# Kernel tuning notes

Measured on AMD Instinct MI355X. Metric: run time of the kernel, lower is better.

The kernel has to match this reference:

```python
import jax, jax.numpy as jnp
import numpy as np

TAU = 2.0
THR = 0.5
ALPHA = 4.0  # Sigmoid_Grad surrogate sharpness
EPS = 1e-5
HEADS = 16
SCALE = 0.25

@jax.custom_vjp
def spike(v):
    return (v > 0.0).astype(v.dtype)

def _spike_fwd(v):
    return (v > 0.0).astype(v.dtype), v

def _spike_bwd(v, g):
    s = jax.nn.sigmoid(ALPHA * v)
    return (g * ALPHA * s * (1.0 - s),)

spike.defvjp(_spike_fwd, _spike_bwd)

def lif(x):
    # x: (T, ...) ; stateful LIF over leading time dim, hard reset (detached spike)
    def step(mem, xt):
        mem = mem + (xt - mem) / TAU
        s = spike(mem - THR)
        mem = mem * (1.0 - jax.lax.stop_gradient(s))
        return mem, s
    _, s = jax.lax.scan(step, jnp.zeros_like(x[0]), x)
    return s

def bn(x, p):
    # x: (T,B,C,N), p: (4,C) = (gamma, beta, mean, var); inference-form BatchNorm1d
    g, b, m, v = p
    shp = (1, 1, -1, 1)
    return (x - m.reshape(shp)) * (g.reshape(shp) / jnp.sqrt(v.reshape(shp) + EPS)) + b.reshape(shp)

def conv_bn_lif(x, w, p, bias=None):
    # 1x1 Conv1d == channel matmul: (T,B,Cin,N) x (Cout,Cin) -> (T,B,Cout,N)
    y = jnp.einsum('tbcn,oc->tbon', x, w)
    if bias is not None:
        y = y + bias.reshape(1, 1, -1, 1)
    return lif(bn(y, p))

def _block(x, q_w, q_bn, k_w, k_bn, v_w, v_bn, proj_w, proj_bn,
           fc1_w, fc1_b, fc1_bn, fc2_w, fc2_b, fc2_bn):
    T, B, C, N = x.shape
    D = C // HEADS

    def to_heads(y):  # (T,B,C,N) -> (T,B,H,N,D)
        return y.transpose(0, 1, 3, 2).reshape(T, B, N, HEADS, D).transpose(0, 1, 3, 2, 4)

    q = to_heads(conv_bn_lif(x, q_w, q_bn))
    k = to_heads(conv_bn_lif(x, k_w, k_bn))
    v = to_heads(conv_bn_lif(x, v_w, v_bn))

    attn = jnp.einsum('tbhnd,tbhmd->tbhnm', q, k) * SCALE  # no softmax
    r = jnp.einsum('tbhnm,tbhmd->tbhnd', attn, v) * SCALE
    r = r.transpose(0, 1, 2, 4, 3).reshape(T, B, C, N)  # (T,B,H,D,N) -> (T,B,C,N)
    r = lif(r)  # attn_lif
    attn_out = conv_bn_lif(r, proj_w, proj_bn)  # proj conv+bn+lif

    x = x + attn_out  # residual 1

    h = conv_bn_lif(x, fc1_w, fc1_bn, fc1_b)
    m = conv_bn_lif(h, fc2_w, fc2_bn, fc2_b)
    return x + m  # residual 2

def setup_inputs() -> dict:
    key = jax.random.key(0)
    ks = jax.random.split(key, 16)
    T, B, C, N = 4, 16, 256, 512
    H = 1024  # mlp hidden = 4*C
    w = 0.05
    d = {}
    d['x'] = jax.random.normal(ks[0], (T, B, C, N), jnp.float32)
    d['q_w'] = jax.random.normal(ks[1], (C, C), jnp.float32) * w
    d['q_bn'] = jax.random.uniform(ks[2], (4, C), jnp.float32, 0.5, 1.5)
    d['k_w'] = jax.random.normal(ks[3], (C, C), jnp.float32) * w
    d['k_bn'] = jax.random.uniform(ks[4], (4, C), jnp.float32, 0.5, 1.5)
    d['v_w'] = jax.random.normal(ks[5], (C, C), jnp.float32) * w
    d['v_bn'] = jax.random.uniform(ks[6], (4, C), jnp.float32, 0.5, 1.5)
    d['proj_w'] = jax.random.normal(ks[7], (C, C), jnp.float32) * w
    d['proj_bn'] = jax.random.uniform(ks[8], (4, C), jnp.float32, 0.5, 1.5)
    d['fc1_w'] = jax.random.normal(ks[9], (H, C), jnp.float32) * w
    d['fc1_b'] = jnp.zeros((H,), jnp.float32)
    d['fc1_bn'] = jax.random.uniform(ks[10], (4, H), jnp.float32, 0.5, 1.5)
    d['fc2_w'] = jax.random.normal(ks[11], (C, H), jnp.float32) * w
    d['fc2_b'] = jnp.zeros((C,), jnp.float32)
    d['fc2_bn'] = jax.random.uniform(ks[12], (4, C), jnp.float32, 0.5, 1.5)
    return d

def reference(x, q_w, q_bn, k_w, k_bn, v_w, v_bn, proj_w, proj_bn,
              fc1_w, fc1_b, fc1_bn, fc2_w, fc2_b, fc2_bn):
    return _block(x, q_w, q_bn, k_w, k_bn, v_w, v_bn, proj_w, proj_bn,
                  fc1_w, fc1_b, fc1_bn, fc2_w, fc2_b, fc2_bn)
```

## Files before the change

kernel.cpp:

```cpp
#include <hip/hip_runtime.h>

#pragma clang fp contract(off)

typedef unsigned char u8;
typedef unsigned int u32;

#define TSTEPS 4

template <int P, int BK, int XMODE, bool HASX2, int OMODE>
__global__ __launch_bounds__(256) void conv_bn_lif(
    const void* __restrict__ X1v, const u8* __restrict__ X2,
    const float* __restrict__ Wt, const float* __restrict__ bias,
    const float* __restrict__ bnp,
    u8* __restrict__ Sout,
    const float* __restrict__ Xres, const u8* __restrict__ AOres,
    float* __restrict__ Fout,
    int Bsz, int Cin, int Cout, int N)
{
  constexpr int BO   = 16 * P;
  constexpr int BN   = 128;
  constexpr int TPR  = 256 / BK;
  constexpr int FPT  = BN / TPR;
  constexpr int NF4  = FPT / 4;
  constexpr int THRO = 256 / BO;
  constexpr int WPAD = (P == 4) ? 4 : 0;
  constexpr int XROWF = BN + 8;

  const int tid = threadIdx.x;
  const int tx = tid & 15, ty = tid >> 4;
  const int nBase = blockIdx.x * BN, oBase = blockIdx.y * BO, b = blockIdx.z;
  const int KT = Cin / BK;
  const int TT = TSTEPS * KT;

  __shared__ __align__(16) float Ws[2][BK][BO + WPAD];
  __shared__ __align__(16) u8 Xraw[(XMODE == 0) ? (2 * BK * XROWF * 4)
                                                : (2 * BK * BN)];
  __shared__ __align__(16) float BnL[BO][4];

  float* XF = (float*)Xraw;
  u8*    X8 = Xraw;

  if (tid < BO) {
    int o = oBase + tid;
    float g  = bnp[0 * Cout + o];
    float be = bnp[1 * Cout + o];
    float m  = bnp[2 * Cout + o];
    float vv = bnp[3 * Cout + o];
    float d_f = (float)((double)vv + (double)1e-5f);
    float s_f = (float)sqrt((double)d_f);
    BnL[tid][0] = (float)((double)g / (double)s_f);
    BnL[tid][1] = m;
    BnL[tid][2] = be;
    BnL[tid][3] = bias ? bias[o] : 0.0f;
  }

  float mem[P][8], acc[P][8];
  #pragma unroll
  for (int p = 0; p < P; ++p)
    #pragma unroll
    for (int q = 0; q < 8; ++q) { mem[p][q] = 0.0f; acc[p][q] = 0.0f; }

  const int xRow = tid / TPR;
  const int xcF  = (tid % TPR) * FPT;
  const int wO   = tid / THRO;
  const int wK   = (tid % THRO) * 8;

  float4 px[NF4];
  u32    pxu[NF4];
  u32    pau[NF4];
  float4 pwa, pwb;

  auto issue = [&](int i) {
    const int tI = i / KT, k0 = (i % KT) * BK;
    const size_t xb = (size_t)(tI * Bsz + b) * Cin * N
                    + (size_t)(k0 + xRow) * N + nBase + xcF;
    if constexpr (XMODE == 0) {
      const float* xp = (const float*)X1v + xb;
      #pragma unroll
      for (int f = 0; f < NF4; ++f) px[f] = *(const float4*)(xp + 4 * f);
    } else {
      const u8* xp = (const u8*)X1v + xb;
      if constexpr (NF4 == 4) {
        uint4 u = *(const uint4*)xp;
        pxu[0] = u.x; pxu[1] = u.y; pxu[2] = u.z; pxu[3] = u.w;
      } else {
        uint2 u = *(const uint2*)xp;
        pxu[0] = u.x; pxu[1] = u.y;
      }
    }
    if constexpr (HASX2) {
      const u8* ap = X2 + xb;
      if constexpr (NF4 == 4) {
        uint4 u = *(const uint4*)ap;
        pau[0] = u.x; pau[1] = u.y; pau[2] = u.z; pau[3] = u.w;
      } else {
        uint2 u = *(const uint2*)ap;
        pau[0] = u.x; pau[1] = u.y;
      }
    }
    const size_t wb = (size_t)(oBase + wO) * Cin + k0 + wK;
    pwa = *(const float4*)(Wt + wb);
    pwb = *(const float4*)(Wt + wb + 4);
  };

  auto commit = [&](int bf) {
    if constexpr (XMODE == 0) {
      #pragma unroll
      for (int f = 0; f < NF4; ++f) {
        float4 v = px[f];
        if constexpr (HASX2) {
          u32 a2 = pau[f];
          v.x = v.x + (float)(a2 & 0xffu);
          v.y = v.y + (float)((a2 >> 8) & 0xffu);
          v.z = v.z + (float)((a2 >> 16) & 0xffu);
          v.w = v.w + (float)((a2 >> 24) & 0xffu);
        }
        *(float4*)&XF[((size_t)(bf * BK + xRow)) * XROWF + xcF + 4 * f] = v;
      }
    } else {
      if constexpr (NF4 == 4) {
        *(uint4*)&X8[(size_t)(bf * BK + xRow) * BN + xcF] =
            make_uint4(pxu[0], pxu[1], pxu[2], pxu[3]);
      } else {
        *(uint2*)&X8[(size_t)(bf * BK + xRow) * BN + xcF] =
            make_uint2(pxu[0], pxu[1]);
      }
    }
    Ws[bf][wK + 0][wO] = pwa.x;  Ws[bf][wK + 1][wO] = pwa.y;
    Ws[bf][wK + 2][wO] = pwa.z;  Ws[bf][wK + 3][wO] = pwa.w;
    Ws[bf][wK + 4][wO] = pwb.x;  Ws[bf][wK + 5][wO] = pwb.y;
    Ws[bf][wK + 6][wO] = pwb.z;  Ws[bf][wK + 7][wO] = pwb.w;
  };

  issue(0);
  commit(0);
  __syncthreads();

  for (int tt = 0; tt < TT; ++tt) {
    const int buf = tt & 1;
    if (tt + 1 < TT) issue(tt + 1);

    #pragma unroll
    for (int kk = 0; kk < BK; ++kk) {
      float xa[8];
      if constexpr (XMODE == 0) {
        float4 x0 = *(const float4*)&XF[(size_t)(buf * BK + kk) * XROWF + tx * 4];
        float4 x1 = *(const float4*)&XF[(size_t)(buf * BK + kk) * XROWF + 64 + tx * 4];
        xa[0] = x0.x; xa[1] = x0.y; xa[2] = x0.z; xa[3] = x0.w;
        xa[4] = x1.x; xa[5] = x1.y; xa[6] = x1.z; xa[7] = x1.w;
      } else {
        uint2 u = *(const uint2*)&X8[(size_t)(buf * BK + kk) * BN + tx * 8];
        #pragma unroll
        for (int j = 0; j < 4; ++j) xa[j]     = (float)((u.x >> (8 * j)) & 0xffu);
        #pragma unroll
        for (int j = 0; j < 4; ++j) xa[4 + j] = (float)((u.y >> (8 * j)) & 0xffu);
      }
      float wa[P];
      float4 w0 = *(const float4*)&Ws[buf][kk][ty * P];
      wa[0] = w0.x; wa[1] = w0.y; wa[2] = w0.z; wa[3] = w0.w;
      if constexpr (P == 8) {
        float4 w1 = *(const float4*)&Ws[buf][kk][ty * P + 4];
        wa[4] = w1.x; wa[5] = w1.y; wa[6] = w1.z; wa[7] = w1.w;
      }
      #pragma unroll
      for (int p = 0; p < P; ++p)
        #pragma unroll
        for (int q = 0; q < 8; ++q)
          acc[p][q] = fmaf(wa[p], xa[q], acc[p][q]);
    }

    if ((tt % KT) == KT - 1) {
      const int t = tt / KT;
      const size_t sbase = (size_t)(t * Bsz + b) * Cout * N;
      #pragma unroll
      for (int p = 0; p < P; ++p) {
        const int o = oBase + ty * P + p;
        float4 bv = *(const float4*)&BnL[ty * P + p][0];
        bool spk[8];
        #pragma unroll
        for (int q = 0; q < 8; ++q) {
          float y = acc[p][q];
          if (bias) y = y + bv.w;
          float t1 = y - bv.y;
          float t2 = t1 * bv.x;
          y = t2 + bv.z;
          float m2 = mem[p][q];
          float dd = y - m2;
          m2 = m2 + dd * 0.5f;
          bool sp = (m2 - 0.5f) > 0.0f;
          mem[p][q] = sp ? 0.0f : m2;
          spk[q] = sp;
          acc[p][q] = 0.0f;
        }
        if constexpr (XMODE == 0) {
          const size_t rb0 = sbase + (size_t)o * N + nBase + tx * 4;
          u32 pk0 = 0, pk1 = 0;
          #pragma unroll
          for (int j = 0; j < 4; ++j) {
            if (spk[j])     pk0 |= (1u << (8 * j));
            if (spk[4 + j]) pk1 |= (1u << (8 * j));
          }
          *(u32*)&Sout[rb0]      = pk0;
          *(u32*)&Sout[rb0 + 64] = pk1;
        } else {
          const size_t rb = sbase + (size_t)o * N + nBase + tx * 8;
          if constexpr (OMODE == 0) {
            u32 pk0 = 0, pk1 = 0;
            #pragma unroll
            for (int j = 0; j < 4; ++j) {
              if (spk[j])     pk0 |= (1u << (8 * j));
              if (spk[4 + j]) pk1 |= (1u << (8 * j));
            }
            *(uint2*)&Sout[rb] = make_uint2(pk0, pk1);
          } else {
            float4 xr0 = *(const float4*)&Xres[rb];
            float4 xr1 = *(const float4*)&Xres[rb + 4];
            uint2 av = *(const uint2*)&AOres[rb];
            float xa4[8] = {xr0.x, xr0.y, xr0.z, xr0.w,
                            xr1.x, xr1.y, xr1.z, xr1.w};
            float o4[8];
            #pragma unroll
            for (int j = 0; j < 4; ++j) {
              float s = spk[j] ? 1.0f : 0.0f;
              float xn = xa4[j] + (float)((av.x >> (8 * j)) & 0xffu);
              o4[j] = xn + s;
            }
            #pragma unroll
            for (int j = 0; j < 4; ++j) {
              float s = spk[4 + j] ? 1.0f : 0.0f;
              float xn = xa4[4 + j] + (float)((av.y >> (8 * j)) & 0xffu);
              o4[4 + j] = xn + s;
            }
            *(float4*)&Fout[rb]     = make_float4(o4[0], o4[1], o4[2], o4[3]);
            *(float4*)&Fout[rb + 4] = make_float4(o4[4], o4[5], o4[6], o4[7]);
          }
        }
      }
    }

    __syncthreads();
    if (tt + 1 < TT) commit((tt + 1) & 1);
    __syncthreads();
  }
}

__global__ __launch_bounds__(256) void attn_lif(
    const u8* __restrict__ Qs, const u8* __restrict__ Ks,
    const u8* __restrict__ Vs, u8* __restrict__ Rs,
    int Bsz, int C, int N)
{
  const int tid = threadIdx.x;
  const int h = blockIdx.x & 15;
  const int b = blockIdx.x >> 4;

  __shared__ u8 qs[16][528];
  __shared__ u8 ks[16][528];
  __shared__ u8 vs[16][528];
  __shared__ int Gs[16][17];

  const int eG = tid >> 4;
  const int dG = tid & 15;
  const int dR = tid >> 4;
  const int nR0 = tid & 15;

  float mem[32];
  #pragma unroll
  for (int i = 0; i < 32; ++i) mem[i] = 0.0f;

  for (int t = 0; t < TSTEPS; ++t) {
    __syncthreads();
    const size_t base = ((size_t)(t * Bsz + b) * C + h * 16) * N;
    for (int i = 0; i < 32; ++i) {
      int flat = tid + 256 * i;
      int d = flat >> 9, n = flat & 511;
      size_t g = base + (size_t)d * N + n;
      qs[d][n] = Qs[g];
      ks[d][n] = Ks[g];
      vs[d][n] = Vs[g];
    }
    __syncthreads();

    int gi = 0;
    for (int n = 0; n < 512; ++n)
      gi += (int)ks[eG][n] * (int)vs[dG][n];
    Gs[eG][dG] = gi;
    __syncthreads();

    int Greg[16];
    #pragma unroll
    for (int e = 0; e < 16; ++e) Greg[e] = Gs[e][dR];

    const size_t obase = ((size_t)(t * Bsz + b) * C + h * 16 + dR) * N;
    for (int j = 0; j < 32; ++j) {
      int n = nR0 + 16 * j;
      int ri = 0;
      #pragma unroll
      for (int e = 0; e < 16; ++e)
        ri += qs[e][n] ? Greg[e] : 0;
      float r = (float)ri * 0.0625f;
      float m2 = mem[j];
      float d = r - m2;
      m2 = m2 + d * 0.5f;
      float s = (m2 - 0.5f) > 0.0f ? 1.0f : 0.0f;
      mem[j] = (s > 0.0f) ? 0.0f : m2;
      Rs[obase + n] = (s > 0.0f) ? (u8)1 : (u8)0;
    }
  }
}

extern "C" void kernel_launch(void* const* d_in, const int* in_sizes, int n_in,
                              void* d_out, int out_size, void* d_ws, size_t ws_size,
                              hipStream_t stream)
{
  const float* x     = (const float*)d_in[0];
  const float* q_w   = (const float*)d_in[1];
  const float* q_bn  = (const float*)d_in[2];
  const float* k_w   = (const float*)d_in[3];
  const float* k_bn  = (const float*)d_in[4];
  const float* v_w   = (const float*)d_in[5];
  const float* v_bn  = (const float*)d_in[6];
  const float* p_w   = (const float*)d_in[7];
  const float* p_bn  = (const float*)d_in[8];
  const float* f1_w  = (const float*)d_in[9];
  const float* f1_b  = (const float*)d_in[10];
  const float* f1_bn = (const float*)d_in[11];
  const float* f2_w  = (const float*)d_in[12];
  const float* f2_b  = (const float*)d_in[13];
  const float* f2_bn = (const float*)d_in[14];

  const int T = 4, B = 16, C = 256, N = 512, Hm = 1024;
  const size_t SZ = (size_t)T * B * C * N;

  char* ws = (char*)d_ws;
  u8* q_s  = (u8*)(ws + 0 * SZ);
  u8* k_s  = (u8*)(ws + 1 * SZ);
  u8* v_s  = (u8*)(ws + 2 * SZ);
  u8* r_s  = (u8*)(ws + 3 * SZ);
  u8* ao_s = (u8*)(ws + 4 * SZ);
  u8* h_s  = (u8*)(ws + 0 * SZ);

  dim3 blk(256);
  dim3 gC64(N / 128, C / 64, B);
  dim3 gF1(N / 128, Hm / 64, B);

  conv_bn_lif<4, 32, 0, false, 0><<<gC64, blk, 0, stream>>>(
      x, nullptr, q_w, nullptr, q_bn, q_s, nullptr, nullptr, nullptr, B, C, C, N);
  conv_bn_lif<4, 32, 0, false, 0><<<gC64, blk, 0, stream>>>(
      x, nullptr, k_w, nullptr, k_bn, k_s, nullptr, nullptr, nullptr, B, C, C, N);
  conv_bn_lif<4, 32, 0, false, 0><<<gC64, blk, 0, stream>>>(
      x, nullptr, v_w, nullptr, v_bn, v_s, nullptr, nullptr, nullptr, B, C, C, N);

  attn_lif<<<dim3(B * 16), blk, 0, stream>>>(q_s, k_s, v_s, r_s, B, C, N);

  conv_bn_lif<4, 32, 1, false, 0><<<gC64, blk, 0, stream>>>(
      r_s, nullptr, p_w, nullptr, p_bn, ao_s, nullptr, nullptr, nullptr, B, C, C, N);
  conv_bn_lif<4, 32, 0, true, 0><<<gF1, blk, 0, stream>>>(
      x, ao_s, f1_w, f1_b, f1_bn, h_s, nullptr, nullptr, nullptr, B, C, Hm, N);
  conv_bn_lif<4, 32, 1, false, 1><<<gC64, blk, 0, stream>>>(
      h_s, nullptr, f2_w, f2_b, f2_bn, nullptr, x, ao_s, (float*)d_out, B, Hm, C, N);
}
```

Measured before the change: 1.050 ms.

## Fuse Q/K/V conv launches and retune per-layer output tile sizes

Merges the three Q, K and V conv+BN+LIF launches into one grid that picks its weight, BN and output pointers from blockIdx.y. This removes two launch gaps and gives the GPU more blocks at once. It also generalises the weight loader so each layer can use its own output-channel tile: P=2 for the proj and fc2 convs to double their block count, and P=8 for fc1 to raise per-thread work. The cost is more template variants, extra runtime pointer selects, and possibly lower arithmetic intensity on the P=2 layers.

```diff
diff --git a/kernel.cpp b/kernel.cpp
--- a/kernel.cpp
+++ b/kernel.cpp
@@ -7,12 +7,14 @@
 
 #define TSTEPS 4
 
-template <int P, int BK, int XMODE, bool HASX2, int OMODE>
+template <int P, int BK, int XMODE, bool HASX2, int OMODE, int NSEL>
 __global__ __launch_bounds__(256) void conv_bn_lif(
     const void* __restrict__ X1v, const u8* __restrict__ X2,
-    const float* __restrict__ Wt, const float* __restrict__ bias,
-    const float* __restrict__ bnp,
-    u8* __restrict__ Sout,
+    const float* __restrict__ W0, const float* __restrict__ W1,
+    const float* __restrict__ W2, const float* __restrict__ bias,
+    const float* __restrict__ bn0, const float* __restrict__ bn1,
+    const float* __restrict__ bn2,
+    u8* __restrict__ S0, u8* __restrict__ S1, u8* __restrict__ S2,
     const float* __restrict__ Xres, const u8* __restrict__ AOres,
     float* __restrict__ Fout,
     int Bsz, int Cin, int Cout, int N)
@@ -22,17 +24,35 @@
   constexpr int TPR  = 256 / BK;
   constexpr int FPT  = BN / TPR;
   constexpr int NF4  = FPT / 4;
-  constexpr int THRO = 256 / BO;
-  constexpr int WPAD = (P == 4) ? 4 : 0;
+  static_assert(NF4 == 4, "loader assumes 16 elems/thread");
+  constexpr int WPT  = BO * BK / 256;
+  constexpr int NW4  = WPT / 4;
+  constexpr int TPW  = BK / WPT;
+  constexpr int WPAD = (P == 4) ? 4 : (P == 2) ? 2 : 0;
+  constexpr int WROW = BO + WPAD;
   constexpr int XROWF = BN + 8;
 
   const int tid = threadIdx.x;
   const int tx = tid & 15, ty = tid >> 4;
-  const int nBase = blockIdx.x * BN, oBase = blockIdx.y * BO, b = blockIdx.z;
+  const int nBase = blockIdx.x * BN, b = blockIdx.z;
+
+  int sel, oBase;
+  if constexpr (NSEL == 3) {
+    const int oT = gridDim.y / 3;
+    sel = blockIdx.y / oT;
+    oBase = (blockIdx.y - sel * oT) * BO;
+  } else {
+    sel = 0;
+    oBase = blockIdx.y * BO;
+  }
+  const float* __restrict__ Wt  = (sel == 0) ? W0 : (sel == 1) ? W1 : W2;
+  const float* __restrict__ bnp = (sel == 0) ? bn0 : (sel == 1) ? bn1 : bn2;
+  u8* __restrict__ Sout         = (sel == 0) ? S0 : (sel == 1) ? S1 : S2;
+
   const int KT = Cin / BK;
   const int TT = TSTEPS * KT;
 
-  __shared__ __align__(16) float Ws[2][BK][BO + WPAD];
+  __shared__ __align__(16) float Ws[2][BK][WROW];
   __shared__ __align__(16) u8 Xraw[(XMODE == 0) ? (2 * BK * XROWF * 4)
                                                 : (2 * BK * BN)];
   __shared__ __align__(16) float BnL[BO][4];
@@ -62,13 +82,13 @@
 
   const int xRow = tid / TPR;
   const int xcF  = (tid % TPR) * FPT;
-  const int wO   = tid / THRO;
-  const int wK   = (tid % THRO) * 8;
+  const int wO   = tid / TPW;
+  const int wK   = (tid % TPW) * WPT;
 
   float4 px[NF4];
   u32    pxu[NF4];
   u32    pau[NF4];
-  float4 pwa, pwb;
+  float4 pw[NW4];
 
   auto issue = [&](int i) {
     const int tI = i / KT, k0 = (i % KT) * BK;
@@ -79,28 +99,16 @@
       #pragma unroll
       for (int f = 0; f < NF4; ++f) px[f] = *(const float4*)(xp + 4 * f);
     } else {
-      const u8* xp = (const u8*)X1v + xb;
-      if constexpr (NF4 == 4) {
-        uint4 u = *(const uint4*)xp;
-        pxu[0] = u.x; pxu[1] = u.y; pxu[2] = u.z; pxu[3] = u.w;
-      } else {
-        uint2 u = *(const uint2*)xp;
-        pxu[0] = u.x; pxu[1] = u.y;
-      }
+      uint4 u = *(const uint4*)((const u8*)X1v + xb);
+      pxu[0] = u.x; pxu[1] = u.y; pxu[2] = u.z; pxu[3] = u.w;
     }
     if constexpr (HASX2) {
-      const u8* ap = X2 + xb;
-      if constexpr (NF4 == 4) {
-        uint4 u = *(const uint4*)ap;
-        pau[0] = u.x; pau[1] = u.y; pau[2] = u.z; pau[3] = u.w;
-      } else {
-        uint2 u = *(const uint2*)ap;
-        pau[0] = u.x; pau[1] = u.y;
-      }
+      uint4 u = *(const uint4*)(X2 + xb);
+      pau[0] = u.x; pau[1] = u.y; pau[2] = u.z; pau[3] = u.w;
     }
     const size_t wb = (size_t)(oBase + wO) * Cin + k0 + wK;
-    pwa = *(const float4*)(Wt + wb);
-    pwb = *(const float4*)(Wt + wb + 4);
+    #pragma unroll
+    for (int f = 0; f < NW4; ++f) pw[f] = *(const float4*)(Wt + wb + 4 * f);
   };
 
   auto commit = [&](int bf) {
@@ -118,18 +126,16 @@
         *(float4*)&XF[((size_t)(bf * BK + xRow)) * XROWF + xcF + 4 * f] = v;
       }
     } else {
-      if constexpr (NF4 == 4) {
-        *(uint4*)&X8[(size_t)(bf * BK + xRow) * BN + xcF] =
-            make_uint4(pxu[0], pxu[1], pxu[2], pxu[3]);
-      } else {
-        *(uint2*)&X8[(size_t)(bf * BK + xRow) * BN + xcF] =
-            make_uint2(pxu[0], pxu[1]);
-      }
-    }
-    Ws[bf][wK + 0][wO] = pwa.x;  Ws[bf][wK + 1][wO] = pwa.y;
-    Ws[bf][wK + 2][wO] = pwa.z;  Ws[bf][wK + 3][wO] = pwa.w;
-    Ws[bf][wK + 4][wO] = pwb.x;  Ws[bf][wK + 5][wO] = pwb.y;
-    Ws[bf][wK + 6][wO] = pwb.z;  Ws[bf][wK + 7][wO] = pwb.w;
+      *(uint4*)&X8[(size_t)(bf * BK + xRow) * BN + xcF] =
+          make_uint4(pxu[0], pxu[1], pxu[2], pxu[3]);
+    }
+    #pragma unroll
+    for (int f = 0; f < NW4; ++f) {
+      Ws[bf][wK + 4 * f + 0][wO] = pw[f].x;
+      Ws[bf][wK + 4 * f + 1][wO] = pw[f].y;
+      Ws[bf][wK + 4 * f + 2][wO] = pw[f].z;
+      Ws[bf][wK + 4 * f + 3][wO] = pw[f].w;
+    }
   };
 
   issue(0);
@@ -156,11 +162,16 @@
         for (int j = 0; j < 4; ++j) xa[4 + j] = (float)((u.y >> (8 * j)) & 0xffu);
       }
       float wa[P];
-      float4 w0 = *(const float4*)&Ws[buf][kk][ty * P];
-      wa[0] = w0.x; wa[1] = w0.y; wa[2] = w0.z; wa[3] = w0.w;
-      if constexpr (P == 8) {
-        float4 w1 = *(const float4*)&Ws[buf][kk][ty * P + 4];
-        wa[4] = w1.x; wa[5] = w1.y; wa[6] = w1.z; wa[7] = w1.w;
+      if constexpr (P == 2) {
+        float2 w0 = *(const float2*)&Ws[buf][kk][ty * 2];
+        wa[0] = w0.x; wa[1] = w0.y;
+      } else {
+        float4 w0 = *(const float4*)&Ws[buf][kk][ty * P];
+        wa[0] = w0.x; wa[1] = w0.y; wa[2] = w0.z; wa[3] = w0.w;
+        if constexpr (P == 8) {
+          float4 w1 = *(const float4*)&Ws[buf][kk][ty * P + 4];
+          wa[4] = w1.x; wa[5] = w1.y; wa[6] = w1.z; wa[7] = w1.w;
+        }
       }
       #pragma unroll
       for (int p = 0; p < P; ++p)
@@ -340,22 +351,23 @@
   u8* h_s  = (u8*)(ws + 0 * SZ);
 
   dim3 blk(256);
-  dim3 gC64(N / 128, C / 64, B);
-  dim3 gF1(N / 128, Hm / 64, B);
-
-  conv_bn_lif<4, 32, 0, false, 0><<<gC64, blk, 0, stream>>>(
-      x, nullptr, q_w, nullptr, q_bn, q_s, nullptr, nullptr, nullptr, B, C, C, N);
-  conv_bn_lif<4, 32, 0, false, 0><<<gC64, blk, 0, stream>>>(
-      x, nullptr, k_w, nullptr, k_bn, k_s, nullptr, nullptr, nullptr, B, C, C, N);
-  conv_bn_lif<4, 32, 0, false, 0><<<gC64, blk, 0, stream>>>(
-      x, nullptr, v_w, nullptr, v_bn, v_s, nullptr, nullptr, nullptr, B, C, C, N);
+  dim3 gQKV(N / 128, 3 * (C / 64), B);
+  dim3 gP2(N / 128, C / 32, B);
+  dim3 gF1(N / 128, Hm / 128, B);
+
+  conv_bn_lif<4, 32, 0, false, 0, 3><<<gQKV, blk, 0, stream>>>(
+      x, nullptr, q_w, k_w, v_w, nullptr, q_bn, k_bn, v_bn,
+      q_s, k_s, v_s, nullptr, nullptr, nullptr, B, C, C, N);
 
   attn_lif<<<dim3(B * 16), blk, 0, stream>>>(q_s, k_s, v_s, r_s, B, C, N);
 
-  conv_bn_lif<4, 32, 1, false, 0><<<gC64, blk, 0, stream>>>(
-      r_s, nullptr, p_w, nullptr, p_bn, ao_s, nullptr, nullptr, nullptr, B, C, C, N);
-  conv_bn_lif<4, 32, 0, true, 0><<<gF1, blk, 0, stream>>>(
-      x, ao_s, f1_w, f1_b, f1_bn, h_s, nullptr, nullptr, nullptr, B, C, Hm, N);
-  conv_bn_lif<4, 32, 1, false, 1><<<gC64, blk, 0, stream>>>(
-      h_s, nullptr, f2_w, f2_b, f2_bn, nullptr, x, ao_s, (float*)d_out, B, Hm, C, N);
+  conv_bn_lif<2, 32, 1, false, 0, 1><<<gP2, blk, 0, stream>>>(
+      r_s, nullptr, p_w, p_w, p_w, nullptr, p_bn, p_bn, p_bn,
+      ao_s, ao_s, ao_s, nullptr, nullptr, nullptr, B, C, C, N);
+  conv_bn_lif<8, 32, 0, true, 0, 1><<<gF1, blk, 0, stream>>>(
+      x, ao_s, f1_w, f1_w, f1_w, f1_b, f1_bn, f1_bn, f1_bn,
+      h_s, h_s, h_s, nullptr, nullptr, nullptr, B, C, Hm, N);
+  conv_bn_lif<2, 32, 1, false, 1, 1><<<gP2, blk, 0, stream>>>(
+      h_s, nullptr, f2_w, f2_w, f2_w, f2_b, f2_bn, f2_bn, f2_bn,
+      nullptr, nullptr, nullptr, x, ao_s, (float*)d_out, B, Hm, C, N);
 }
```

After: 985.1 us. 6.2% less time.
